# Optimization experiments

Hardware: AMD Instinct MI355X
Metric: run time of the kernel (lower is better)

The kernel has to match this reference:

```python
import jax, jax.numpy as jnp
import numpy as np

B, S, D, H, M, E, K = 4, 2048, 1024, 2048, 64, 8, 2  # batch, seq, d_model, max_neurons, moe_hidden, experts, top_k


def setup_inputs() -> dict:
    key = jax.random.key(0)
    ks = jax.random.split(key, 10)
    r = lambda k, shape: jax.random.normal(k, shape, dtype=jnp.float32) * 0.02
    return {
        "inputs_embeds": jax.random.normal(ks[0], (B, S, D), dtype=jnp.float32),
        "enc_W": r(ks[1], (D, H)), "enc_b": jnp.zeros((H,), jnp.float32),
        "s2c_W": r(ks[2], (H, M)), "s2c_b": jnp.zeros((M,), jnp.float32),
        "rW1": r(ks[3], (M, 64)), "rb1": jnp.zeros((64,), jnp.float32),
        "rW2": r(ks[4], (64, E)), "rb2": jnp.zeros((E,), jnp.float32),
        "We1": r(ks[5], (E, M, H // 2)), "be1": jnp.zeros((E, H // 2), jnp.float32),
        "We2": r(ks[6], (E, H // 2, M)), "be2": jnp.zeros((E, M), jnp.float32),
        "c2s_W": r(ks[7], (M, H)), "c2s_b": jnp.zeros((H,), jnp.float32),
        "dec_W": r(ks[8], (H, D)), "dec_b": jnp.zeros((D,), jnp.float32),
        "ln_g": jnp.ones((D,), jnp.float32), "ln_b": jnp.zeros((D,), jnp.float32),
    }


def _layernorm(x, g, b, eps=1e-5):
    mu = x.mean(-1, keepdims=True)
    var = ((x - mu) ** 2).mean(-1, keepdims=True)
    return (x - mu) * jax.lax.rsqrt(var + eps) * g + b


def _forward(inputs_embeds, enc_W, enc_b, s2c_W, s2c_b, rW1, rb1, rW2, rb2,
             We1, be1, We2, be2, c2s_W, c2s_b, dec_W, dec_b, ln_g, ln_b):
    b, s, _ = inputs_embeds.shape
    # GIFNeuron encoder (rate-coded surrogate spikes)
    spikes_enc = jax.nn.sigmoid(inputs_embeds @ enc_W + enc_b)          # (B,S,H)
    flat = spikes_enc.reshape(b * s, H)                                  # (N,H)
    # SpikeToContinuousBridge ('rate'): projection to MoE hidden
    cont = flat @ s2c_W + s2c_b                                          # (N,M)
    # LiquidMoERouter: 2-layer router, softmax, top-k, renormalize
    logits = jnp.tanh(cont @ rW1 + rb1) @ rW2 + rb2                      # (N,E)
    probs = jax.nn.softmax(logits, axis=-1)
    topw, topi = jax.lax.top_k(probs, K)                                 # (N,K)
    w = topw / topw.sum(-1, keepdims=True)
    # dense per-token per-expert gate == sum_k weights[:,k] * (indices[:,k]==e)
    gates = (jax.nn.one_hot(topi, E, dtype=cont.dtype) * w[..., None]).sum(1)  # (N,E)
    # SNNExpert MLP per expert, dense dispatch + weighted combine (index_add equivalent)
    h = jax.nn.relu(jnp.einsum('nm,emh->enh', cont, We1) + be1[:, None, :])    # (E,N,H/2)
    expert_out = jnp.einsum('enh,ehm->enm', h, We2) + be2[:, None, :]          # (E,N,M)
    output_flat = jnp.einsum('enm,ne->nm', expert_out, gates)                  # (N,M)
    # ContinuousToSpikeBridge ('poisson', expected rate), 2D -> 1 timestep
    spikes_moe = jax.nn.sigmoid(output_flat @ c2s_W + c2s_b).reshape(b, s, H)
    # GIFNeuron decoder + LayerNorm
    decoded = jax.nn.sigmoid(spikes_moe @ dec_W + dec_b)                 # (B,S,D)
    return _layernorm(decoded, ln_g, ln_b)


def reference(inputs_embeds, enc_W, enc_b, s2c_W, s2c_b, rW1, rb1, rW2, rb2,
              We1, be1, We2, be2, c2s_W, c2s_b, dec_W, dec_b, ln_g, ln_b):
    return _forward(inputs_embeds, enc_W, enc_b, s2c_W, s2c_b, rW1, rb1, rW2, rb2,
                    We1, be1, We2, be2, c2s_W, c2s_b, dec_W, dec_b, ln_g, ln_b)
```

## Files before the change

kernel.cpp:

```cpp
#include <hip/hip_runtime.h>
#include <hip/hip_bf16.h>
#include <cstdint>
#include <cstddef>

#define TOK    8192
#define DMODEL 1024
#define HDIM   2048
#define MDIM   64
#define NEXP   8
#define HHALF  1024

using f32x4  = __attribute__((ext_vector_type(4))) float;
using bf16x8 = __attribute__((ext_vector_type(8))) __bf16;
using bf16x4 = __attribute__((ext_vector_type(4))) __bf16;

__device__ __forceinline__ void async16(const void* g, void* l) {
  __builtin_amdgcn_global_load_lds(
      (const __attribute__((address_space(1))) unsigned int*)g,
      (__attribute__((address_space(3))) unsigned int*)l, 16, 0, 0);
}
__device__ __forceinline__ void wait_vm6() { asm volatile("s_waitcnt vmcnt(6)" ::: "memory"); }
__device__ __forceinline__ void wait_vm0() { asm volatile("s_waitcnt vmcnt(0)" ::: "memory"); }

__global__ __launch_bounds__(256) void preamble_kernel(
    const float* __restrict__ X, __bf16* __restrict__ Xb,
    const float* __restrict__ encW, __bf16* __restrict__ encWT,
    const float* __restrict__ s2cW, __bf16* __restrict__ s2cWT,
    const float* __restrict__ c2sW, __bf16* __restrict__ c2sWT,
    const float* __restrict__ decW, __bf16* __restrict__ decWT,
    const float* __restrict__ We1, __bf16* __restrict__ We1T,
    const float* __restrict__ We2, __bf16* __restrict__ We2T) {
  __shared__ float ts[32][33];
  const int tid = threadIdx.x;
  int b = blockIdx.x;
  if (b < 8192) {
    int i = b * 256 + tid;
    float4 v = ((const float4*)X)[i];
    bf16x4 o = { (__bf16)v.x, (__bf16)v.y, (__bf16)v.z, (__bf16)v.w };
    ((bf16x4*)Xb)[i] = o;
    return;
  }
  b -= 8192;
  const float* in; __bf16* outp; int R, C, tx, ty;
  if (b < 2048)              { in = encW; outp = encWT; R = 1024; C = 2048; tx = b % 64; ty = b / 64; }
  else if ((b -= 2048) < 128){ in = s2cW; outp = s2cWT; R = 2048; C = 64;   tx = b % 2;  ty = b / 2;  }
  else if ((b -= 128) < 128) { in = c2sW; outp = c2sWT; R = 64;   C = 2048; tx = b % 64; ty = b / 64; }
  else if ((b -= 128) < 2048){ in = decW; outp = decWT; R = 2048; C = 1024; tx = b % 32; ty = b / 32; }
  else if ((b -= 2048) < 512){ int s = b / 64, t = b % 64;
                               in = We1 + (size_t)s * 65536; outp = We1T + (size_t)s * 65536;
                               R = 64; C = 1024; tx = t % 32; ty = t / 32; }
  else                       { b -= 512; int s = b / 64, t = b % 64;
                               in = We2 + (size_t)s * 65536; outp = We2T + (size_t)s * 65536;
                               R = 1024; C = 64; tx = t % 2; ty = t / 2; }
  const int c0 = tx * 32, r0 = ty * 32;
  const int x = tid & 31, y = tid >> 5;
  #pragma unroll
  for (int i = y; i < 32; i += 8) ts[i][x] = in[(size_t)(r0 + i) * C + c0 + x];
  __syncthreads();
  #pragma unroll
  for (int i = y; i < 32; i += 8)
    outp[(size_t)(c0 + i) * R + r0 + x] = (__bf16)ts[x][i];
}
#define PREAMBLE_BLOCKS (8192 + 2048 + 128 + 128 + 2048 + 512 + 512)

template <int BM, int BN, int WAVES, int OUT_BF16, int ACT, int BIAS, int SUMA>
__global__ __launch_bounds__(WAVES * 64) void gemm_bt(
    const __bf16* __restrict__ A, const __bf16* __restrict__ Bt,
    const float* __restrict__ bias, void* __restrict__ Cout,
    int M, int N, int K, const __bf16* __restrict__ A2) {
  constexpr int BK = 64;
  constexpr int WAVES_N = WAVES / 2;
  constexpr int WTM = BM / 32;
  constexpr int WTN = BN / (WAVES_N * 16);
  constexpr int NBUF = SUMA ? 1 : 3;
  constexpr int A_ISSUES = BM / (8 * WAVES);
  constexpr int B_ISSUES = BN / (8 * WAVES);
  static_assert(SUMA || (A_ISSUES + B_ISSUES == 6), "vmcnt literal assumes 6 loads/stage");
  __shared__ __bf16 As[NBUF * BM * BK];
  __shared__ __bf16 Bs[NBUF * BN * BK];
  const int tid = threadIdx.x;
  const int wave = tid >> 6, lane = tid & 63;
  const int quad = lane >> 4, l16 = lane & 15;
  const int m0 = blockIdx.x * BM, n0 = blockIdx.y * BN;
  const int ks = K / gridDim.z;
  const int kbeg = blockIdx.z * ks;
  const int wm = (wave & 1) * (BM / 2);
  const int wn = (wave >> 1) * (BN / WAVES_N);
  const int lrow = lane >> 3;
  const int lchunk = lane & 7;
  f32x4 acc[WTM][WTN] = {};

  const __bf16* aSrc[A_ISSUES];
  const __bf16* bSrc[B_ISSUES];
  #pragma unroll
  for (int t = 0; t < A_ISSUES; ++t) {
    int row = (t * WAVES + wave) * 8 + lrow;
    aSrc[t] = A + (size_t)(m0 + row) * K + kbeg + (lchunk ^ (row & 7)) * 8;
  }
  #pragma unroll
  for (int t = 0; t < B_ISSUES; ++t) {
    int row = (t * WAVES + wave) * 8 + lrow;
    bSrc[t] = Bt + (size_t)(n0 + row) * K + kbeg + (lchunk ^ (row & 7)) * 8;
  }
  int aOff[WTM][2], bOff[WTN][2];
  #pragma unroll
  for (int i = 0; i < WTM; ++i) {
    int row = wm + i * 16 + l16;
    #pragma unroll
    for (int kk = 0; kk < 2; ++kk)
      aOff[i][kk] = row * BK + (((kk * 4 + quad) ^ (row & 7)) * 8);
  }
  #pragma unroll
  for (int j = 0; j < WTN; ++j) {
    int row = wn + j * 16 + l16;
    #pragma unroll
    for (int kk = 0; kk < 2; ++kk)
      bOff[j][kk] = row * BK + (((kk * 4 + quad) ^ (row & 7)) * 8);
  }

  auto stage = [&](__bf16* Ad, __bf16* Bd) {
    #pragma unroll
    for (int t = 0; t < A_ISSUES; ++t) {
      async16(aSrc[t], Ad + (t * WAVES + wave) * 8 * BK);
      aSrc[t] += BK;
    }
    #pragma unroll
    for (int t = 0; t < B_ISSUES; ++t) {
      async16(bSrc[t], Bd + (t * WAVES + wave) * 8 * BK);
      bSrc[t] += BK;
    }
  };
  auto compute = [&](const __bf16* Ab, const __bf16* Bb) {
    #pragma unroll
    for (int kk = 0; kk < 2; ++kk) {
      bf16x8 af[WTM], bfr[WTN];
      #pragma unroll
      for (int i = 0; i < WTM; ++i) af[i] = *(const bf16x8*)(Ab + aOff[i][kk]);
      #pragma unroll
      for (int j = 0; j < WTN; ++j) bfr[j] = *(const bf16x8*)(Bb + bOff[j][kk]);
      #pragma unroll
      for (int i = 0; i < WTM; ++i)
        #pragma unroll
        for (int j = 0; j < WTN; ++j)
          acc[i][j] = __builtin_amdgcn_mfma_f32_16x16x32_bf16(af[i], bfr[j], acc[i][j], 0, 0, 0);
    }
  };

  const int niter = ks / BK;
  if constexpr (SUMA) {
    for (int it = 0; it < niter; ++it) {
      __syncthreads();
      #pragma unroll
      for (int t = 0; t < A_ISSUES; ++t) {
        int row = (t * WAVES + wave) * 8 + lrow;
        size_t go = (size_t)(m0 + row) * K + kbeg + it * BK + lchunk * 8;
        bf16x8 a0 = *(const bf16x8*)(A + go);
        bf16x8 a1 = *(const bf16x8*)(A2 + go);
        bf16x8 s;
        #pragma unroll
        for (int q = 0; q < 8; ++q) s[q] = (__bf16)((float)a0[q] + (float)a1[q]);
        *(bf16x8*)(As + row * BK + ((lchunk ^ (row & 7)) * 8)) = s;
      }
      #pragma unroll
      for (int t = 0; t < B_ISSUES; ++t) {
        async16(bSrc[t], Bs + (t * WAVES + wave) * 8 * BK);
        bSrc[t] += BK;
      }
      __syncthreads();
      compute(As, Bs);
    }
  } else {
    __bf16* a0 = As;  __bf16* a1 = As + BM * BK;  __bf16* a2 = As + 2 * BM * BK;
    __bf16* b0 = Bs;  __bf16* b1 = Bs + BN * BK;  __bf16* b2 = Bs + 2 * BN * BK;
    stage(a0, b0);
    if (niter > 1) stage(a1, b1);
    for (int it = 0; it < niter; ++it) {
      if (it + 1 < niter) wait_vm6(); else wait_vm0();
      __builtin_amdgcn_s_barrier();
      if (it + 2 < niter) stage(a2, b2);
      compute(a0, b0);
      __bf16* t;
      t = a0; a0 = a1; a1 = a2; a2 = t;
      t = b0; b0 = b1; b1 = b2; b2 = t;
    }
  }

  char* Cz = (char*)Cout + (size_t)blockIdx.z * M * N * (OUT_BF16 ? 2 : 4);
  #pragma unroll
  for (int i = 0; i < WTM; ++i)
    #pragma unroll
    for (int j = 0; j < WTN; ++j)
      #pragma unroll
      for (int r = 0; r < 4; ++r) {
        int m = m0 + wm + i * 16 + quad * 4 + r;
        int n = n0 + wn + j * 16 + l16;
        float v = acc[i][j][r];
        if (BIAS) v += bias[n];
        if (ACT == 1) v = 1.0f / (1.0f + __expf(-v));
        if (OUT_BF16)
          ((__bf16*)Cz)[(size_t)m * N + n] = (__bf16)v;
        else
          ((float*)Cz)[(size_t)m * N + n] = v;
      }
}

__global__ __launch_bounds__(256) void router_kernel(
    const float* __restrict__ contP, const float* __restrict__ s2c_b,
    const float* __restrict__ rW1, const float* __restrict__ rb1,
    const float* __restrict__ rW2, const float* __restrict__ rb2,
    __bf16* __restrict__ contB, int* __restrict__ e01,
    float2* __restrict__ g01) {
  const int wave = threadIdx.x >> 6, lane = threadIdx.x & 63;
  const int n = blockIdx.x * 4 + wave;
  const size_t base = (size_t)n * 64 + lane;
  const size_t slab = (size_t)TOK * 64;
  float c = contP[base] + contP[base + slab] + contP[base + 2 * slab] +
            contP[base + 3 * slab] + s2c_b[lane];
  contB[base] = (__bf16)c;
  float acc = rb1[lane];
  #pragma unroll
  for (int i = 0; i < 64; ++i) {
    float ci = __shfl(c, i);
    acc = fmaf(ci, rW1[i * 64 + lane], acc);
  }
  float t = tanhf(acc);
  float logit[8];
  #pragma unroll
  for (int e = 0; e < 8; ++e) {
    float v = t * rW2[lane * 8 + e];
    #pragma unroll
    for (int o = 32; o; o >>= 1) v += __shfl_xor(v, o);
    logit[e] = v + rb2[e];
  }
  float mx = logit[0];
  #pragma unroll
  for (int e = 1; e < 8; ++e) mx = fmaxf(mx, logit[e]);
  float p[8];
  #pragma unroll
  for (int e = 0; e < 8; ++e) p[e] = __expf(logit[e] - mx);
  float v0 = p[0]; int e0 = 0;
  #pragma unroll
  for (int e = 1; e < 8; ++e) if (p[e] > v0) { v0 = p[e]; e0 = e; }
  float v1 = -1.0f; int e1 = 0;
  #pragma unroll
  for (int e = 0; e < 8; ++e) if (e != e0 && p[e] > v1) { v1 = p[e]; e1 = e; }
  float inv = 1.0f / (v0 + v1);
  if (lane == 0) {
    e01[n] = e0 | (e1 << 8);
    g01[n] = make_float2(v0 * inv, v1 * inv);
  }
}

__global__ __launch_bounds__(256) void moe_fused_kernel(
    const __bf16* __restrict__ contB, const __bf16* __restrict__ We1T,
    const __bf16* __restrict__ We2T, const float* __restrict__ be1,
    const float* __restrict__ be2, const int* __restrict__ e01,
    const float2* __restrict__ g01, __bf16* __restrict__ slab0,
    __bf16* __restrict__ slab1) {
  constexpr int TT = 128;
  const int e = blockIdx.y;
  const int t0 = blockIdx.x * TT;
  __shared__ __bf16 cont_s[TT * 64];
  __shared__ __bf16 w1_s[64 * 64];
  __shared__ __bf16 w2_s[64 * 64];
  __shared__ __bf16 h_s[TT * 64];
  __shared__ int   e01_s[TT];
  __shared__ float g0_s[TT], g1_s[TT];
  const int tid = threadIdx.x;
  const int wave = tid >> 6, lane = tid & 63;
  const int quad = lane >> 4, l16 = lane & 15;
  if (tid < TT) {
    e01_s[tid] = e01[t0 + tid];
    float2 g = g01[t0 + tid];
    g0_s[tid] = g.x; g1_s[tid] = g.y;
  }
  for (int i = tid; i < TT * 8; i += 256) {
    int r = i >> 3, cc = i & 7;
    *(uint4*)(cont_s + r * 64 + ((cc ^ (r & 7)) * 8)) =
        *(const uint4*)(contB + (size_t)(t0 + r) * 64 + cc * 8);
  }
  const int wtok = wave * 32;
  f32x4 acc2[2][4] = {};
  for (int hc = 0; hc < HHALF; hc += 64) {
    __syncthreads();
    for (int c = tid; c < 512; c += 256) {
      int r = c >> 3, cc = c & 7;
      *(uint4*)(w1_s + r * 64 + ((cc ^ (r & 7)) * 8)) =
          *(const uint4*)(We1T + ((size_t)e * HHALF + hc + r) * 64 + cc * 8);
      *(uint4*)(w2_s + r * 64 + ((cc ^ (r & 7)) * 8)) =
          *(const uint4*)(We2T + ((size_t)e * 64 + r) * HHALF + hc + cc * 8);
    }
    __syncthreads();
    f32x4 acc1[2][4] = {};
    #pragma unroll
    for (int kk = 0; kk < 2; ++kk) {
      bf16x8 af[2], bfr[4];
      #pragma unroll
      for (int i = 0; i < 2; ++i) {
        int row = wtok + i * 16 + l16;
        af[i] = *(const bf16x8*)(cont_s + row * 64 + (((kk * 4 + quad) ^ (row & 7)) * 8));
      }
      #pragma unroll
      for (int j = 0; j < 4; ++j) {
        int row = j * 16 + l16;
        bfr[j] = *(const bf16x8*)(w1_s + row * 64 + (((kk * 4 + quad) ^ (row & 7)) * 8));
      }
      #pragma unroll
      for (int i = 0; i < 2; ++i)
        #pragma unroll
        for (int j = 0; j < 4; ++j)
          acc1[i][j] = __builtin_amdgcn_mfma_f32_16x16x32_bf16(af[i], bfr[j], acc1[i][j], 0, 0, 0);
    }
    #pragma unroll
    for (int i = 0; i < 2; ++i)
      #pragma unroll
      for (int j = 0; j < 4; ++j)
        #pragma unroll
        for (int r = 0; r < 4; ++r) {
          int tr = wtok + i * 16 + quad * 4 + r;
          int hcol = j * 16 + l16;
          float v = acc1[i][j][r] + be1[e * HHALF + hc + hcol];
          h_s[tr * 64 + (((hcol >> 3) ^ (tr & 7)) * 8) + (hcol & 7)] =
              (__bf16)fmaxf(v, 0.0f);
        }
    #pragma unroll
    for (int kk = 0; kk < 2; ++kk) {
      bf16x8 af[2], bfr[4];
      #pragma unroll
      for (int i = 0; i < 2; ++i) {
        int row = wtok + i * 16 + l16;
        af[i] = *(const bf16x8*)(h_s + row * 64 + (((kk * 4 + quad) ^ (row & 7)) * 8));
      }
      #pragma unroll
      for (int j = 0; j < 4; ++j) {
        int row = j * 16 + l16;
        bfr[j] = *(const bf16x8*)(w2_s + row * 64 + (((kk * 4 + quad) ^ (row & 7)) * 8));
      }
      #pragma unroll
      for (int i = 0; i < 2; ++i)
        #pragma unroll
        for (int j = 0; j < 4; ++j)
          acc2[i][j] = __builtin_amdgcn_mfma_f32_16x16x32_bf16(af[i], bfr[j], acc2[i][j], 0, 0, 0);
    }
  }
  #pragma unroll
  for (int i = 0; i < 2; ++i)
    #pragma unroll
    for (int j = 0; j < 4; ++j)
      #pragma unroll
      for (int r = 0; r < 4; ++r) {
        int tr = wtok + i * 16 + quad * 4 + r;
        int m = j * 16 + l16;
        int pe = e01_s[tr];
        size_t o = (size_t)(t0 + tr) * 64 + m;
        if ((pe & 0xff) == e)
          slab0[o] = (__bf16)(g0_s[tr] * (acc2[i][j][r] + be2[e * 64 + m]));
        else if (((pe >> 8) & 0xff) == e)
          slab1[o] = (__bf16)(g1_s[tr] * (acc2[i][j][r] + be2[e * 64 + m]));
      }
}

__global__ __launch_bounds__(256) void ln_kernel(
    const float* __restrict__ x, const float* __restrict__ g,
    const float* __restrict__ b, float* __restrict__ out) {
  const int row = blockIdx.x;
  const float4 v = ((const float4*)(x + (size_t)row * 1024))[threadIdx.x];
  float s1 = v.x + v.y + v.z + v.w;
  float s2 = v.x * v.x + v.y * v.y + v.z * v.z + v.w * v.w;
  #pragma unroll
  for (int o = 32; o; o >>= 1) { s1 += __shfl_xor(s1, o); s2 += __shfl_xor(s2, o); }
  __shared__ float ws1[4], ws2[4];
  const int wave = threadIdx.x >> 6, lane = threadIdx.x & 63;
  if (lane == 0) { ws1[wave] = s1; ws2[wave] = s2; }
  __syncthreads();
  s1 = ws1[0] + ws1[1] + ws1[2] + ws1[3];
  s2 = ws2[0] + ws2[1] + ws2[2] + ws2[3];
  const float mu = s1 * (1.0f / 1024.0f);
  const float var = s2 * (1.0f / 1024.0f) - mu * mu;
  const float inv = rsqrtf(var + 1e-5f);
  const int col = threadIdx.x * 4;
  const float4 gv = *(const float4*)(g + col);
  const float4 bv = *(const float4*)(b + col);
  float4 o;
  o.x = (v.x - mu) * inv * gv.x + bv.x;
  o.y = (v.y - mu) * inv * gv.y + bv.y;
  o.z = (v.z - mu) * inv * gv.z + bv.z;
  o.w = (v.w - mu) * inv * gv.w + bv.w;
  *(float4*)(out + (size_t)row * 1024 + col) = o;
}

extern "C" void kernel_launch(void* const* d_in, const int* in_sizes, int n_in,
                              void* d_out, int out_size, void* d_ws, size_t ws_size,
                              hipStream_t stream) {
  const float* X     = (const float*)d_in[0];
  const float* enc_W = (const float*)d_in[1];
  const float* enc_b = (const float*)d_in[2];
  const float* s2c_W = (const float*)d_in[3];
  const float* s2c_b = (const float*)d_in[4];
  const float* rW1   = (const float*)d_in[5];
  const float* rb1   = (const float*)d_in[6];
  const float* rW2   = (const float*)d_in[7];
  const float* rb2   = (const float*)d_in[8];
  const float* We1   = (const float*)d_in[9];
  const float* be1   = (const float*)d_in[10];
  const float* We2   = (const float*)d_in[11];
  const float* be2   = (const float*)d_in[12];
  const float* c2s_W = (const float*)d_in[13];
  const float* c2s_b = (const float*)d_in[14];
  const float* dec_W = (const float*)d_in[15];
  const float* dec_b = (const float*)d_in[16];
  const float* ln_g  = (const float*)d_in[17];
  const float* ln_b  = (const float*)d_in[18];
  float* out = (float*)d_out;

  char* ws = (char*)d_ws;
  size_t off = 0;
  auto take = [&](size_t bytes) -> char* {
    char* p = ws + off;
    off = (off + bytes + 255) & ~(size_t)255;
    return p;
  };
  const size_t SLAB = (size_t)TOK * HDIM * 2;
  char*   slabA     = take(SLAB);
  char*   slabB     = take(SLAB);
  __bf16* encWT     = (__bf16*)take((size_t)HDIM * DMODEL * 2);
  __bf16* s2cWT     = (__bf16*)take((size_t)MDIM * HDIM * 2);
  __bf16* c2sWT     = (__bf16*)take((size_t)HDIM * MDIM * 2);
  __bf16* decWT     = (__bf16*)take((size_t)DMODEL * HDIM * 2);
  __bf16* We1T      = (__bf16*)take((size_t)NEXP * HHALF * MDIM * 2);
  __bf16* We2T      = (__bf16*)take((size_t)NEXP * MDIM * HHALF * 2);
  __bf16* contB     = (__bf16*)take((size_t)TOK * MDIM * 2);
  int*    e01       = (int*)take((size_t)TOK * 4);
  float2* g01       = (float2*)take((size_t)TOK * 8);
  __bf16* oslab0    = (__bf16*)take((size_t)TOK * MDIM * 2);
  __bf16* oslab1    = (__bf16*)take((size_t)TOK * MDIM * 2);
  if (off > ws_size) return;

  __bf16* Xb        = (__bf16*)slabA;
  float*  contP     = (float*)(slabA + (size_t)TOK * DMODEL * 2);
  __bf16* spikesMoe = (__bf16*)slabA;
  __bf16* spikesEnc = (__bf16*)slabB;
  float*  decoded   = (float*)slabB;

  preamble_kernel<<<PREAMBLE_BLOCKS, 256, 0, stream>>>(
      X, Xb, enc_W, encWT, s2c_W, s2cWT, c2s_W, c2sWT, dec_W, decWT,
      We1, We1T, We2, We2T);

  gemm_bt<128, 256, 8, 1, 1, 1, 0><<<dim3(TOK / 128, HDIM / 256, 1), 512, 0, stream>>>(
      Xb, encWT, enc_b, spikesEnc, TOK, HDIM, DMODEL, nullptr);
  gemm_bt<128, 64, 4, 0, 0, 0, 0><<<dim3(TOK / 128, 1, 4), 256, 0, stream>>>(
      spikesEnc, s2cWT, nullptr, contP, TOK, MDIM, HDIM, nullptr);
  router_kernel<<<TOK / 4, 256, 0, stream>>>(contP, s2c_b, rW1, rb1, rW2, rb2,
                                             contB, e01, g01);
  moe_fused_kernel<<<dim3(TOK / 128, NEXP), 256, 0, stream>>>(
      contB, We1T, We2T, be1, be2, e01, g01, oslab0, oslab1);
  gemm_bt<128, 128, 4, 1, 1, 1, 1><<<dim3(TOK / 128, HDIM / 128, 1), 256, 0, stream>>>(
      oslab0, c2sWT, c2s_b, spikesMoe, TOK, HDIM, MDIM, oslab1);
  gemm_bt<128, 256, 8, 0, 1, 1, 0><<<dim3(TOK / 128, DMODEL / 256, 1), 512, 0, stream>>>(
      spikesMoe, decWT, dec_b, decoded, TOK, DMODEL, HDIM, nullptr);
  ln_kernel<<<TOK, 256, 0, stream>>>(decoded, ln_g, ln_b, out);
}
```

Before: 322.8 us.

## Add 256-row-tile GEMM with interleaved MFMA/LDS schedule for encoder and decoder

Introduces a new gemm_mt kernel using BM=256 tiles where each wave computes a 128x64 subtile, with LDS fragment loads interleaved between MFMA groups, s_setprio raising and extra barriers, and double or triple buffered async global-to-LDS loads. The encoder GEMM uses 256x256 tiles with 8 waves and 2 buffers; the decoder GEMM uses 256x128 tiles with 4 waves and 3 buffers. Larger tiles raise arithmetic intensity and cut redundant operand loads. In exchange the accumulators grow to 8x4 fragments per wave, which raises register pressure, and the grids get fewer blocks.

```diff
diff --git a/kernel.cpp b/kernel.cpp
--- a/kernel.cpp
+++ b/kernel.cpp
@@ -19,8 +19,6 @@
       (const __attribute__((address_space(1))) unsigned int*)g,
       (__attribute__((address_space(3))) unsigned int*)l, 16, 0, 0);
 }
-__device__ __forceinline__ void wait_vm6() { asm volatile("s_waitcnt vmcnt(6)" ::: "memory"); }
-__device__ __forceinline__ void wait_vm0() { asm volatile("s_waitcnt vmcnt(0)" ::: "memory"); }
 
 __global__ __launch_bounds__(256) void preamble_kernel(
     const float* __restrict__ X, __bf16* __restrict__ Xb,
@@ -62,6 +60,163 @@
     outp[(size_t)(c0 + i) * R + r0 + x] = (__bf16)ts[x][i];
 }
 #define PREAMBLE_BLOCKS (8192 + 2048 + 128 + 128 + 2048 + 512 + 512)
+
+template <int BN, int WAVES, int NBUF, int OUT_BF16, int ACT, int BIAS>
+__global__ __launch_bounds__(WAVES * 64, WAVES == 8 ? 2 : 1) void gemm_mt(
+    const __bf16* __restrict__ A, const __bf16* __restrict__ Bt,
+    const float* __restrict__ bias, void* __restrict__ Cout,
+    int M, int N, int K) {
+  constexpr int BM = 256, BK = 64;
+  constexpr int A_ISSUES = BM / (8 * WAVES);
+  constexpr int B_ISSUES = BN / (8 * WAVES);
+  constexpr int LOADS = A_ISSUES + B_ISSUES;
+  static_assert((NBUF == 2 && LOADS == 8) || (NBUF == 3 && LOADS == 12),
+                "vmcnt literals assume LOADS=8 (NBUF2) or 12 (NBUF3)");
+  __shared__ __bf16 As[NBUF * BM * BK];
+  __shared__ __bf16 Bs[NBUF * BN * BK];
+  const int tid = threadIdx.x;
+  const int wave = tid >> 6, lane = tid & 63;
+  const int quad = lane >> 4, l16 = lane & 15;
+  const int m0 = blockIdx.x * BM, n0 = blockIdx.y * BN;
+  const int wm = (wave & 1) * 128;
+  const int wn = (wave >> 1) * 64;
+  const int lrow = lane >> 3, lchunk = lane & 7;
+  f32x4 acc[8][4] = {};
+
+  const __bf16* aSrc[A_ISSUES];
+  const __bf16* bSrc[B_ISSUES];
+  #pragma unroll
+  for (int t = 0; t < A_ISSUES; ++t) {
+    int row = (t * WAVES + wave) * 8 + lrow;
+    aSrc[t] = A + (size_t)(m0 + row) * K + (lchunk ^ (row & 7)) * 8;
+  }
+  #pragma unroll
+  for (int t = 0; t < B_ISSUES; ++t) {
+    int row = (t * WAVES + wave) * 8 + lrow;
+    bSrc[t] = Bt + (size_t)(n0 + row) * K + (lchunk ^ (row & 7)) * 8;
+  }
+  int aOff[8], bOff[4];
+  #pragma unroll
+  for (int rf = 0; rf < 8; ++rf) {
+    int row = wm + rf * 16 + l16;
+    aOff[rf] = row * BK + ((quad ^ (row & 7)) * 8);
+  }
+  #pragma unroll
+  for (int cf = 0; cf < 4; ++cf) {
+    int row = wn + cf * 16 + l16;
+    bOff[cf] = row * BK + ((quad ^ (row & 7)) * 8);
+  }
+
+  auto stage = [&](__bf16* Ad, __bf16* Bd) {
+    #pragma unroll
+    for (int t = 0; t < A_ISSUES; ++t) {
+      async16(aSrc[t], Ad + (t * WAVES + wave) * 8 * BK);
+      aSrc[t] += BK;
+    }
+    #pragma unroll
+    for (int t = 0; t < B_ISSUES; ++t) {
+      async16(bSrc[t], Bd + (t * WAVES + wave) * 8 * BK);
+      bSrc[t] += BK;
+    }
+  };
+
+  __bf16 *cA0 = As, *cA1 = As + BM * BK, *cA2 = As + 2 * BM * BK;
+  __bf16 *cB0 = Bs, *cB1 = Bs + BN * BK, *cB2 = Bs + 2 * BN * BK;
+  const int nt = K / BK;
+  stage(cA0, cB0);
+  if constexpr (NBUF == 3) stage(cA1, cB1);
+
+  for (int t = 0; t < nt; ++t) {
+    if constexpr (NBUF == 2) {
+      if (t + 1 < nt) stage(cA1, cB1);
+    } else {
+      if (t + 2 < nt) stage(cA2, cB2);
+    }
+    const int ahead = nt - 1 - t;
+    if constexpr (NBUF == 2) {
+      if (ahead >= 1) asm volatile("s_waitcnt vmcnt(8)" ::: "memory");
+      else            asm volatile("s_waitcnt vmcnt(0)" ::: "memory");
+    } else {
+      if (ahead >= 2)      asm volatile("s_waitcnt vmcnt(24)" ::: "memory");
+      else if (ahead == 1) asm volatile("s_waitcnt vmcnt(12)" ::: "memory");
+      else                 asm volatile("s_waitcnt vmcnt(0)" ::: "memory");
+    }
+    asm volatile("s_barrier" ::: "memory");
+
+    bf16x8 af[4], ag[4], bv[4], bw[4];
+    #pragma unroll
+    for (int r = 0; r < 4; ++r) af[r] = *(const bf16x8*)(cA0 + aOff[r]);
+    #pragma unroll
+    for (int c = 0; c < 4; ++c) bv[c] = *(const bf16x8*)(cB0 + bOff[c]);
+    #pragma unroll
+    for (int r = 0; r < 4; ++r) ag[r] = *(const bf16x8*)(cA0 + aOff[4 + r]);
+    __builtin_amdgcn_s_setprio(1);
+    #pragma unroll
+    for (int c = 0; c < 4; ++c)
+      #pragma unroll
+      for (int r = 0; r < 4; ++r)
+        acc[r][c] = __builtin_amdgcn_mfma_f32_16x16x32_bf16(af[r], bv[c], acc[r][c], 0, 0, 0);
+    __builtin_amdgcn_s_setprio(0);
+    asm volatile("s_barrier" ::: "memory");
+    #pragma unroll
+    for (int r = 0; r < 4; ++r) af[r] = *(const bf16x8*)(cA0 + (aOff[r] ^ 32));
+    #pragma unroll
+    for (int c = 0; c < 4; ++c) bw[c] = *(const bf16x8*)(cB0 + (bOff[c] ^ 32));
+    __builtin_amdgcn_s_setprio(1);
+    #pragma unroll
+    for (int c = 0; c < 4; ++c)
+      #pragma unroll
+      for (int r = 0; r < 4; ++r)
+        acc[4 + r][c] = __builtin_amdgcn_mfma_f32_16x16x32_bf16(ag[r], bv[c], acc[4 + r][c], 0, 0, 0);
+    __builtin_amdgcn_s_setprio(0);
+    asm volatile("s_barrier" ::: "memory");
+    #pragma unroll
+    for (int r = 0; r < 4; ++r) ag[r] = *(const bf16x8*)(cA0 + (aOff[4 + r] ^ 32));
+    __builtin_amdgcn_s_setprio(1);
+    #pragma unroll
+    for (int c = 0; c < 4; ++c)
+      #pragma unroll
+      for (int r = 0; r < 4; ++r)
+        acc[r][c] = __builtin_amdgcn_mfma_f32_16x16x32_bf16(af[r], bw[c], acc[r][c], 0, 0, 0);
+    __builtin_amdgcn_s_setprio(0);
+    asm volatile("s_barrier" ::: "memory");
+    __builtin_amdgcn_s_setprio(1);
+    #pragma unroll
+    for (int c = 0; c < 4; ++c)
+      #pragma unroll
+      for (int r = 0; r < 4; ++r)
+        acc[4 + r][c] = __builtin_amdgcn_mfma_f32_16x16x32_bf16(ag[r], bw[c], acc[4 + r][c], 0, 0, 0);
+    __builtin_amdgcn_s_setprio(0);
+    asm volatile("s_barrier" ::: "memory");
+
+    if constexpr (NBUF == 2) {
+      __bf16* x;
+      x = cA0; cA0 = cA1; cA1 = x;
+      x = cB0; cB0 = cB1; cB1 = x;
+    } else {
+      __bf16* x;
+      x = cA0; cA0 = cA1; cA1 = cA2; cA2 = x;
+      x = cB0; cB0 = cB1; cB1 = cB2; cB2 = x;
+    }
+  }
+
+  #pragma unroll
+  for (int rf = 0; rf < 8; ++rf)
+    #pragma unroll
+    for (int cf = 0; cf < 4; ++cf)
+      #pragma unroll
+      for (int r = 0; r < 4; ++r) {
+        int m = m0 + wm + rf * 16 + quad * 4 + r;
+        int n = n0 + wn + cf * 16 + l16;
+        float v = acc[rf][cf][r];
+        if (BIAS) v += bias[n];
+        if (ACT == 1) v = 1.0f / (1.0f + __expf(-v));
+        if (OUT_BF16)
+          ((__bf16*)Cout)[(size_t)m * N + n] = (__bf16)v;
+        else
+          ((float*)Cout)[(size_t)m * N + n] = v;
+      }
+}
 
 template <int BM, int BN, int WAVES, int OUT_BF16, int ACT, int BIAS, int SUMA>
 __global__ __launch_bounds__(WAVES * 64) void gemm_bt(
@@ -175,7 +330,8 @@
     stage(a0, b0);
     if (niter > 1) stage(a1, b1);
     for (int it = 0; it < niter; ++it) {
-      if (it + 1 < niter) wait_vm6(); else wait_vm0();
+      if (it + 1 < niter) asm volatile("s_waitcnt vmcnt(6)" ::: "memory");
+      else                asm volatile("s_waitcnt vmcnt(0)" ::: "memory");
       __builtin_amdgcn_s_barrier();
       if (it + 2 < niter) stage(a2, b2);
       compute(a0, b0);
@@ -446,8 +602,8 @@
       X, Xb, enc_W, encWT, s2c_W, s2cWT, c2s_W, c2sWT, dec_W, decWT,
       We1, We1T, We2, We2T);
 
-  gemm_bt<128, 256, 8, 1, 1, 1, 0><<<dim3(TOK / 128, HDIM / 256, 1), 512, 0, stream>>>(
-      Xb, encWT, enc_b, spikesEnc, TOK, HDIM, DMODEL, nullptr);
+  gemm_mt<256, 8, 2, 1, 1, 1><<<dim3(TOK / 256, HDIM / 256), 512, 0, stream>>>(
+      Xb, encWT, enc_b, spikesEnc, TOK, HDIM, DMODEL);
   gemm_bt<128, 64, 4, 0, 0, 0, 0><<<dim3(TOK / 128, 1, 4), 256, 0, stream>>>(
       spikesEnc, s2cWT, nullptr, contP, TOK, MDIM, HDIM, nullptr);
   router_kernel<<<TOK / 4, 256, 0, stream>>>(contP, s2c_b, rW1, rb1, rW2, rb2,
@@ -456,7 +612,7 @@
       contB, We1T, We2T, be1, be2, e01, g01, oslab0, oslab1);
   gemm_bt<128, 128, 4, 1, 1, 1, 1><<<dim3(TOK / 128, HDIM / 128, 1), 256, 0, stream>>>(
       oslab0, c2sWT, c2s_b, spikesMoe, TOK, HDIM, MDIM, oslab1);
-  gemm_bt<128, 256, 8, 0, 1, 1, 0><<<dim3(TOK / 128, DMODEL / 256, 1), 512, 0, stream>>>(
-      spikesMoe, decWT, dec_b, decoded, TOK, DMODEL, HDIM, nullptr);
+  gemm_mt<128, 4, 3, 0, 1, 1><<<dim3(TOK / 256, DMODEL / 128), 256, 0, stream>>>(
+      spikesMoe, decWT, dec_b, decoded, TOK, DMODEL, HDIM);
   ln_kernel<<<TOK, 256, 0, stream>>>(decoded, ln_g, ln_b, out);
 }
```

After: 320.3 us. Within noise of the previous version (-0.8%).
